# Performance work log

Hardware: AMD Instinct MI355X
Metric: run time of the kernel (lower is better)

The kernel has to match this reference:

```python
import jax, jax.numpy as jnp
import numpy as np

B, N, HID, HEADS, LAYERS, POOL = 2, 2048, 256, 4, 2, 128
D = HID // HEADS  # per-head dim


def attn_pool(x, w1, b1, w2, b2):
    # x: [B,N,HID]; mask is all-ones in this module's forward, so plain softmax
    s = jnp.tanh(x @ w1 + b1) @ w2 + b2            # [B,N]
    a = jax.nn.softmax(s, axis=-1)                  # [B,N]
    return jnp.einsum('bn,bnc->bc', a, x)           # [B,HID]


def gat_layer(x, adj_mask, proj_w, a_src, a_dst):
    # x: [B,N,HID] -> h: [B,N,HEADS,D]
    h = (x @ proj_w).reshape(x.shape[0], x.shape[1], HEADS, D)
    src = jnp.einsum('bnhd,hd->bnh', h, a_src)      # [B,N,H]
    dst = jnp.einsum('bnhd,hd->bnh', h, a_dst)      # [B,N,H]
    logits = src[:, :, None, :] + dst[:, None, :, :]  # [B,i,j,H]
    logits = jnp.where(logits >= 0, logits, 0.2 * logits)  # leaky_relu(0.2)
    logits = jnp.where(adj_mask[..., None], logits, jnp.float32(-1e9))
    attn = jax.nn.softmax(logits, axis=2)           # softmax over j (neighbors)
    out = jnp.einsum('bijh,bjhd->bihd', attn, h)
    return out.reshape(x.shape[0], x.shape[1], HEADS * D)


def setup_inputs() -> dict:
    key = jax.random.key(0)
    ks = jax.random.split(key, 16)
    sd = 0.05
    gene_expr = jax.random.normal(ks[0], (B, N), dtype=jnp.float32)
    gene_adj = jax.random.randint(ks[1], (B, N, N), 0, 2, dtype=jnp.int32)
    in_w = jax.random.normal(ks[2], (HID,), dtype=jnp.float32) * sd
    in_b = jax.random.normal(ks[3], (HID,), dtype=jnp.float32) * sd
    proj_w = jax.random.normal(ks[4], (LAYERS, HID, HID), dtype=jnp.float32) * sd
    attn_src = jax.random.normal(ks[5], (LAYERS, HEADS, D), dtype=jnp.float32) * sd
    attn_dst = jax.random.normal(ks[6], (LAYERS, HEADS, D), dtype=jnp.float32) * sd
    pool_w1 = jax.random.normal(ks[7], (LAYERS, HID, POOL), dtype=jnp.float32) * sd
    pool_b1 = jax.random.normal(ks[8], (LAYERS, POOL), dtype=jnp.float32) * sd
    pool_w2 = jax.random.normal(ks[9], (LAYERS, POOL), dtype=jnp.float32) * sd
    pool_b2 = jax.random.normal(ks[10], (LAYERS,), dtype=jnp.float32) * sd
    ip_w1 = jax.random.normal(ks[11], (HID, POOL), dtype=jnp.float32) * sd
    ip_b1 = jax.random.normal(ks[12], (POOL,), dtype=jnp.float32) * sd
    ip_w2 = jax.random.normal(ks[13], (POOL,), dtype=jnp.float32) * sd
    ip_b2 = jax.random.normal(ks[14], (), dtype=jnp.float32) * sd
    return dict(gene_expr=gene_expr, gene_adj=gene_adj, in_w=in_w, in_b=in_b,
                proj_w=proj_w, attn_src=attn_src, attn_dst=attn_dst,
                pool_w1=pool_w1, pool_b1=pool_b1, pool_w2=pool_w2, pool_b2=pool_b2,
                ip_w1=ip_w1, ip_b1=ip_b1, ip_w2=ip_w2, ip_b2=ip_b2)


def reference(gene_expr, gene_adj, in_w, in_b, proj_w, attn_src, attn_dst,
              pool_w1, pool_b1, pool_w2, pool_b2, ip_w1, ip_b1, ip_w2, ip_b2):
    # input_proj: Linear(1, HID) on gene_expr[...,None], then relu
    x = jax.nn.relu(gene_expr[:, :, None] * in_w + in_b)  # [B,N,HID]
    raw_pooled = attn_pool(x, ip_w1, ip_b1, ip_w2, ip_b2)
    adj_mask = gene_adj > 0
    node_outs, pooled_outs = [], []
    cur = x
    for l in range(LAYERS):
        cur = gat_layer(cur, adj_mask, proj_w[l], attn_src[l], attn_dst[l])
        cur = jax.nn.elu(cur)
        node_outs.append(cur)
        pooled_outs.append(attn_pool(cur, pool_w1[l], pool_b1[l], pool_w2[l], pool_b2[l]))
    # (raw_pooled, node_out_0, node_out_1, pooled_0, pooled_1); final_pooled == pooled_outs[-1]
    return (raw_pooled, *node_outs, *pooled_outs)
```

## Files before the change

### kernel.cpp

```cpp
#include <hip/hip_runtime.h>
#include <hip/hip_bf16.h>

#define B_ 2
#define N_ 2048
#define HID_ 256
#define HEADS_ 4
#define D_ 64
#define POOL_ 128
#define LOG2E_ 1.4426950408889634f

typedef __bf16 bf16;
typedef __bf16 bf16x8 __attribute__((ext_vector_type(8)));
typedef float f32x4 __attribute__((ext_vector_type(4)));

__device__ __forceinline__ float fast_tanh(float x) {
    x = fminf(fmaxf(x, -15.f), 15.f);
    float t = __expf(2.f * x);
    return (t - 1.f) / (t + 1.f);
}

__global__ void k_setup(const int* __restrict__ adj, unsigned* __restrict__ am,
                        const float* __restrict__ ge, const float* __restrict__ iw,
                        const float* __restrict__ ib, bf16* __restrict__ xb,
                        const float* __restrict__ proj_w, const float* __restrict__ ipw1,
                        const float* __restrict__ pw1, bf16* __restrict__ wT0,
                        bf16* __restrict__ wT1, bf16* __restrict__ ipw1T,
                        bf16* __restrict__ w1T0, bf16* __restrict__ w1T1) {
    int blk = blockIdx.x, tid = threadIdx.x;
    if (blk < 32768) {
        int gid = blk * 256 + tid;
        int v = adj[gid];
        unsigned long long mask = __ballot(v > 0);
        int lane = tid & 63;
        if (lane == 0) am[gid >> 5] = (unsigned)mask;
        else if (lane == 32) am[gid >> 5] = (unsigned)(mask >> 32);
    } else if (blk < 36864) {
        int row = blk - 32768;
        float g = ge[row];
        float v = fmaxf(g * iw[tid] + ib[tid], 0.f);
        xb[row * HID_ + tid] = (bf16)v;
    } else {
        int o = (blk - 36864) * 256 + tid;
        const float* src; bf16* dst; int Nc, loc;
        if (o < 65536)       { src = proj_w;         dst = wT0;   Nc = 256; loc = o; }
        else if (o < 131072) { src = proj_w + 65536; dst = wT1;   Nc = 256; loc = o - 65536; }
        else if (o < 163840) { src = ipw1;           dst = ipw1T; Nc = 128; loc = o - 131072; }
        else if (o < 196608) { src = pw1;            dst = w1T0;  Nc = 128; loc = o - 163840; }
        else                 { src = pw1 + 32768;    dst = w1T1;  Nc = 128; loc = o - 196608; }
        int n = loc >> 8, k = loc & 255;
        dst[loc] = (bf16)src[k * Nc + n];
    }
}

__device__ __forceinline__ void pool_sw_body(const bf16* __restrict__ A,
                                             const bf16* __restrict__ W1T,
                                             const float* __restrict__ b1,
                                             const float* __restrict__ w2,
                                             const float* __restrict__ b2,
                                             float* __restrict__ part,
                                             float* __restrict__ pz,
                                             int slot, int b, int ch, char* smemraw) {
    int n0 = ch * 16;
    int tid = threadIdx.x;
    int w = tid >> 6, lane = tid & 63, r = lane & 15, g = lane >> 4;
    const bf16* ap = A + ((long long)(b * N_ + n0) + r) * 256 + g * 8;
    f32x4 acc[2] = {{0,0,0,0},{0,0,0,0}};
    for (int ks = 0; ks < 256; ks += 32) {
        bf16x8 af = *(const bf16x8*)(ap + ks);
        #pragma unroll
        for (int nf = 0; nf < 2; ++nf) {
            bf16x8 bfr = *(const bf16x8*)(W1T + (w * 32 + nf * 16 + r) * 256 + ks + g * 8);
            acc[nf] = __builtin_amdgcn_mfma_f32_16x16x32_bf16(af, bfr, acc[nf], 0, 0, 0);
        }
    }
    float b1v[2], w2v[2];
    #pragma unroll
    for (int nf = 0; nf < 2; ++nf) {
        b1v[nf] = b1[w * 32 + nf * 16 + r];
        w2v[nf] = w2[w * 32 + nf * 16 + r];
    }
    float (*pred)[16] = (float (*)[16])smemraw;
    float* el = (float*)(smemraw + 256);
    #pragma unroll
    for (int q = 0; q < 4; ++q) {
        float p = fast_tanh(acc[0][q] + b1v[0]) * w2v[0] + fast_tanh(acc[1][q] + b1v[1]) * w2v[1];
        p += __shfl_xor(p, 1); p += __shfl_xor(p, 2);
        p += __shfl_xor(p, 4); p += __shfl_xor(p, 8);
        if (r == 0) pred[w][g * 4 + q] = p;
    }
    __syncthreads();
    if (tid < 16) {
        float s = pred[0][tid] + pred[1][tid] + pred[2][tid] + pred[3][tid] + b2[0];
        el[tid] = __expf(s);
    }
    __syncthreads();
    if (tid == 0) {
        float z = 0.f;
        #pragma unroll
        for (int n = 0; n < 16; ++n) z += el[n];
        pz[(slot * B_ + b) * 128 + ch] = z;
    }
    const bf16* xp = A + (long long)(b * N_ + n0) * 256 + tid;
    float accum = 0.f;
    #pragma unroll
    for (int n = 0; n < 16; ++n) accum += el[n] * (float)xp[n * 256];
    part[(((long long)slot * B_ + b) * 128 + ch) * 256 + tid] = accum;
}

__global__ __launch_bounds__(256) void k_gemm_h_pool(const bf16* __restrict__ A,
                                                     const bf16* __restrict__ WT,
                                                     const float* __restrict__ as,
                                                     const float* __restrict__ ad,
                                                     bf16* __restrict__ hbT,
                                                     float* __restrict__ srcM,
                                                     float* __restrict__ dstT,
                                                     const bf16* __restrict__ W1T,
                                                     const float* __restrict__ b1,
                                                     const float* __restrict__ w2,
                                                     const float* __restrict__ b2,
                                                     float* __restrict__ part,
                                                     float* __restrict__ pz, int slot) {
    __shared__ __align__(16) char smem[16640];
    int blk = blockIdx.x;
    if (blk >= 256) {
        int pb = blk - 256;
        pool_sw_body(A, W1T, b1, w2, b2, part, pz, slot, pb >> 7, pb & 127, smem);
        return;
    }
    int i0 = (blk & 63) * 64, hd = blk >> 6;
    int n0 = hd * 64;
    int w = threadIdx.x >> 6, lane = threadIdx.x & 63, r = lane & 15, g = lane >> 4;
    const bf16* ap = A + (i0 + w * 16 + r) * 256 + g * 8;
    f32x4 acc[4] = {{0,0,0,0},{0,0,0,0},{0,0,0,0},{0,0,0,0}};
    for (int ks = 0; ks < 256; ks += 32) {
        bf16x8 af = *(const bf16x8*)(ap + ks);
        #pragma unroll
        for (int nf = 0; nf < 4; ++nf) {
            bf16x8 bfr = *(const bf16x8*)(WT + (n0 + nf * 16 + r) * 256 + ks + g * 8);
            acc[nf] = __builtin_amdgcn_mfma_f32_16x16x32_bf16(af, bfr, acc[nf], 0, 0, 0);
        }
    }
    int b = i0 >> 11, nbase = i0 & 2047;
    int bh = b * HEADS_ + hd;
    float asv[4], adv[4];
    #pragma unroll
    for (int nf = 0; nf < 4; ++nf) {
        asv[nf] = as[hd * 64 + nf * 16 + r] * LOG2E_;
        adv[nf] = ad[hd * 64 + nf * 16 + r] * LOG2E_;
    }
    float (*tr)[65] = (float (*)[65])smem;
    #pragma unroll
    for (int q = 0; q < 4; ++q) {
        int ln = w * 16 + g * 4 + q;
        float ps = 0.f, pd = 0.f;
        #pragma unroll
        for (int nf = 0; nf < 4; ++nf) {
            float v = acc[nf][q];
            ps += v * asv[nf];
            pd += v * adv[nf];
            tr[nf * 16 + r][ln] = v;
        }
        ps += __shfl_xor(ps, 1); ps += __shfl_xor(ps, 2);
        ps += __shfl_xor(ps, 4); ps += __shfl_xor(ps, 8);
        pd += __shfl_xor(pd, 1); pd += __shfl_xor(pd, 2);
        pd += __shfl_xor(pd, 4); pd += __shfl_xor(pd, 8);
        if (r == 0) {
            srcM[bh * N_ + nbase + ln] = ps;
            dstT[bh * N_ + nbase + ln] = pd;
        }
    }
    __syncthreads();
    int ld = threadIdx.x >> 2, ln0 = (threadIdx.x & 3) * 16;
    bf16x8 o0, o1;
    #pragma unroll
    for (int e = 0; e < 8; ++e) {
        o0[e] = (bf16)tr[ld][ln0 + e];
        o1[e] = (bf16)tr[ld][ln0 + 8 + e];
    }
    bf16* hp = hbT + ((long long)bh * D_ + ld) * N_ + nbase + ln0;
    *(bf16x8*)(hp) = o0;
    *(bf16x8*)(hp + 8) = o1;
}

__global__ __launch_bounds__(256) void k_pool_sw(const bf16* __restrict__ A,
                                                 const bf16* __restrict__ W1T,
                                                 const float* __restrict__ b1,
                                                 const float* __restrict__ w2,
                                                 const float* __restrict__ b2,
                                                 float* __restrict__ part,
                                                 float* __restrict__ pz, int slot) {
    __shared__ __align__(16) char smem[320];
    pool_sw_body(A, W1T, b1, w2, b2, part, pz, slot, blockIdx.y, blockIdx.x, smem);
}

__global__ __launch_bounds__(512, 4) void k_attn(const float* __restrict__ srcM,
                                                 const float* __restrict__ dstT,
                                                 const unsigned* __restrict__ am,
                                                 const bf16* __restrict__ hbT,
                                                 float* __restrict__ nodeOut,
                                                 bf16* __restrict__ xbNext) {
    int it = blockIdx.x, hd = blockIdx.y, b = blockIdx.z;
    int i0 = it * 32;
    int tid = threadIdx.x;
    int w = tid >> 6, lane = tid & 63, r = lane & 15, g = lane >> 4;
    int rg = w >> 2, wj = w & 3;
    int bh = b * HEADS_ + hd;
    const float* drow = dstT + bh * N_;
    const bf16* vbase = hbT + (long long)bh * D_ * N_;

    __shared__ __align__(16) char smem[34816];
    bf16* vt = (bf16*)smem;
    float (*accs)[16][68] = (float (*)[16][68])smem;
    __shared__ float lred[8][16];

    int i = i0 + rg * 16 + r;
    const unsigned* mrow = am + ((long long)(b * N_ + i)) * 64;
    float sv = srcM[bh * N_ + i];

    f32x4 acc[4] = {{0,0,0,0},{0,0,0,0},{0,0,0,0},{0,0,0,0}};
    float l = 0.f;

    bf16x8 st[4];
    #pragma unroll
    for (int k = 0; k < 4; ++k) {
        int s = tid + k * 512, d = s >> 5, seg = s & 31;
        st[k] = *(const bf16x8*)(vbase + d * N_ + seg * 8);
    }

    #pragma unroll
    for (int t = 0; t < 8; ++t) {
        #pragma unroll
        for (int k = 0; k < 4; ++k) {
            int s = tid + k * 512, d = s >> 5, seg = s & 31;
            *(bf16x8*)(vt + d * 264 + seg * 8) = st[k];
        }
        __syncthreads();
        if (t < 7) {
            #pragma unroll
            for (int k = 0; k < 4; ++k) {
                int s = tid + k * 512, d = s >> 5, seg = s & 31;
                st[k] = *(const bf16x8*)(vbase + d * N_ + (t + 1) * 256 + seg * 8);
            }
        }
        #pragma unroll
        for (int s = 0; s < 2; ++s) {
            int jb = t * 256 + wj * 64 + s * 32 + g * 8;
            float4 dv0 = *(const float4*)(drow + jb);
            float4 dv1 = *(const float4*)(drow + jb + 4);
            unsigned mb = (mrow[t * 8 + wj * 2 + s] >> (g * 8)) & 0xFFu;
            float dd[8] = {dv0.x, dv0.y, dv0.z, dv0.w, dv1.x, dv1.y, dv1.z, dv1.w};
            bf16x8 af;
            float es[8];
            #pragma unroll
            for (int tt = 0; tt < 8; ++tt) {
                float s2 = sv + dd[tt];
                float lv = fmaxf(s2, 0.2f * s2);
                float e2 = exp2f(lv);
                e2 = ((mb >> tt) & 1u) ? e2 : 0.f;
                es[tt] = e2;
                af[tt] = (bf16)e2;
            }
            l += ((es[0] + es[1]) + (es[2] + es[3])) + ((es[4] + es[5]) + (es[6] + es[7]));
            #pragma unroll
            for (int nf = 0; nf < 4; ++nf) {
                bf16x8 vf = *(const bf16x8*)(vt + (nf * 16 + r) * 264 + wj * 64 + s * 32 + g * 8);
                acc[nf] = __builtin_amdgcn_mfma_f32_16x16x32_bf16(af, vf, acc[nf], 0, 0, 0);
            }
        }
        __syncthreads();
    }

    l += __shfl_xor(l, 16);
    l += __shfl_xor(l, 32);
    if (g == 0) lred[w][r] = l;
    #pragma unroll
    for (int nf = 0; nf < 4; ++nf)
        #pragma unroll
        for (int q = 0; q < 4; ++q)
            accs[w][g * 4 + q][nf * 16 + r] = acc[nf][q];
    __syncthreads();

    int cc = lane;
    #pragma unroll
    for (int k = 0; k < 4; ++k) {
        int rr = w * 4 + k;
        int rg2 = rr >> 4, rl = rr & 15;
        float ls = 0.f, v = 0.f;
        #pragma unroll
        for (int w2 = 0; w2 < 4; ++w2) {
            ls += lred[rg2 * 4 + w2][rl];
            v += accs[rg2 * 4 + w2][rl][cc];
        }
        v /= ls;
        float o = v > 0.f ? v : expm1f(v);
        int idx = (b * N_ + i0 + rr) * HID_ + hd * D_ + cc;
        nodeOut[idx] = o;
        xbNext[idx] = (bf16)o;
    }
}

__global__ __launch_bounds__(256) void k_pool_finals(const float* __restrict__ part,
                                                     const float* __restrict__ pz,
                                                     float* __restrict__ outRaw,
                                                     float* __restrict__ pool0,
                                                     float* __restrict__ pool1) {
    int slot = blockIdx.x >> 1, b = blockIdx.x & 1;
    int tid = threadIdx.x;
    int lane = tid & 63, w = tid >> 6;
    float z = (tid < 128) ? pz[(slot * B_ + b) * 128 + tid] : 0.f;
    #pragma unroll
    for (int o = 1; o < 64; o <<= 1) z += __shfl_xor(z, o);
    __shared__ float red[4];
    if (lane == 0) red[w] = z;
    __syncthreads();
    float Z = red[0] + red[1] + red[2] + red[3];
    float acc = 0.f;
    #pragma unroll 8
    for (int ch = 0; ch < 128; ++ch)
        acc += part[(((long long)slot * B_ + b) * 128 + ch) * 256 + tid];
    float* out = slot == 0 ? outRaw : (slot == 1 ? pool0 : pool1);
    out[b * HID_ + tid] = acc / Z;
}

extern "C" void kernel_launch(void* const* d_in, const int* in_sizes, int n_in,
                              void* d_out, int out_size, void* d_ws, size_t ws_size,
                              hipStream_t stream) {
    const float* ge     = (const float*)d_in[0];
    const int*   adj    = (const int*)d_in[1];
    const float* in_w   = (const float*)d_in[2];
    const float* in_b   = (const float*)d_in[3];
    const float* proj_w = (const float*)d_in[4];
    const float* a_src  = (const float*)d_in[5];
    const float* a_dst  = (const float*)d_in[6];
    const float* pw1    = (const float*)d_in[7];
    const float* pb1    = (const float*)d_in[8];
    const float* pw2    = (const float*)d_in[9];
    const float* pb2    = (const float*)d_in[10];
    const float* ipw1   = (const float*)d_in[11];
    const float* ipb1   = (const float*)d_in[12];
    const float* ipw2   = (const float*)d_in[13];
    const float* ipb2   = (const float*)d_in[14];

    char* ws = (char*)d_ws;
    bf16*     xb    = (bf16*)(ws + 0);
    bf16*     hbT   = (bf16*)(ws + 2097152);
    float*    srcM  = (float*)(ws + 4194304);
    float*    dstT  = (float*)(ws + 4259840);
    unsigned* am    = (unsigned*)(ws + 4325376);
    bf16*     wT0   = (bf16*)(ws + 5373952);
    bf16*     wT1   = wT0 + 65536;
    bf16*     ipw1T = wT1 + 65536;
    bf16*     w1T0  = ipw1T + 32768;
    bf16*     w1T1  = w1T0 + 32768;
    float*    part  = (float*)(ws + 5832704);
    float*    pz    = (float*)(ws + 6619136);

    float* outRaw = (float*)d_out;
    float* node0  = outRaw + 512;
    float* node1  = node0 + 1048576;
    float* pool0  = node1 + 1048576;
    float* pool1  = pool0 + 512;

    k_setup<<<37760, 256, 0, stream>>>(adj, am, ge, in_w, in_b, xb,
                                       proj_w, ipw1, pw1, wT0, wT1, ipw1T, w1T0, w1T1);

    k_gemm_h_pool<<<512, 256, 0, stream>>>(xb, wT0, a_src, a_dst, hbT, srcM, dstT,
                                           ipw1T, ipb1, ipw2, ipb2, part, pz, 0);
    k_attn<<<dim3(64, 4, 2), 512, 0, stream>>>(srcM, dstT, am, hbT, node0, xb);

    k_gemm_h_pool<<<512, 256, 0, stream>>>(xb, wT1, a_src + 256, a_dst + 256, hbT, srcM, dstT,
                                           w1T0, pb1, pw2, pb2, part, pz, 1);
    k_attn<<<dim3(64, 4, 2), 512, 0, stream>>>(srcM, dstT, am, hbT, node1, xb);

    k_pool_sw<<<dim3(128, B_), 256, 0, stream>>>(xb, w1T1, pb1 + POOL_, pw2 + 1, pb2 + 1,
                                                 part, pz, 2);
    k_pool_finals<<<6, 256, 0, stream>>>(part, pz, outRaw, pool0, pool1);
}
```

Baseline: 111.4 us.

## Restructure GAT attention: 16-row blocks, per-wave j-split, direct global V loads

```diff
diff --git a/kernel.cpp b/kernel.cpp
--- a/kernel.cpp
+++ b/kernel.cpp
@@ -193,85 +193,68 @@
     pool_sw_body(A, W1T, b1, w2, b2, part, pz, slot, blockIdx.y, blockIdx.x, smem);
 }
 
-__global__ __launch_bounds__(512, 4) void k_attn(const float* __restrict__ srcM,
+__global__ __launch_bounds__(512, 8) void k_attn(const float* __restrict__ srcM,
                                                  const float* __restrict__ dstT,
                                                  const unsigned* __restrict__ am,
                                                  const bf16* __restrict__ hbT,
                                                  float* __restrict__ nodeOut,
                                                  bf16* __restrict__ xbNext) {
     int it = blockIdx.x, hd = blockIdx.y, b = blockIdx.z;
-    int i0 = it * 32;
+    int i0 = it * 16;
     int tid = threadIdx.x;
     int w = tid >> 6, lane = tid & 63, r = lane & 15, g = lane >> 4;
-    int rg = w >> 2, wj = w & 3;
     int bh = b * HEADS_ + hd;
     const float* drow = dstT + bh * N_;
     const bf16* vbase = hbT + (long long)bh * D_ * N_;
 
     __shared__ __align__(16) char smem[34816];
-    bf16* vt = (bf16*)smem;
+    float* dls = (float*)smem;
     float (*accs)[16][68] = (float (*)[16][68])smem;
     __shared__ float lred[8][16];
 
-    int i = i0 + rg * 16 + r;
-    const unsigned* mrow = am + ((long long)(b * N_ + i)) * 64;
+    *(float4*)(dls + tid * 4) = *(const float4*)(drow + tid * 4);
+
+    int i = i0 + r;
+    const unsigned* mrow = am + ((long long)(b * N_ + i)) * 64 + w * 8;
+    uint4 m0 = *(const uint4*)(mrow);
+    uint4 m1 = *(const uint4*)(mrow + 4);
+    unsigned mw[8] = {m0.x, m0.y, m0.z, m0.w, m1.x, m1.y, m1.z, m1.w};
     float sv = srcM[bh * N_ + i];
 
     f32x4 acc[4] = {{0,0,0,0},{0,0,0,0},{0,0,0,0},{0,0,0,0}};
     float l = 0.f;
-
-    bf16x8 st[4];
-    #pragma unroll
-    for (int k = 0; k < 4; ++k) {
-        int s = tid + k * 512, d = s >> 5, seg = s & 31;
-        st[k] = *(const bf16x8*)(vbase + d * N_ + seg * 8);
-    }
-
-    #pragma unroll
-    for (int t = 0; t < 8; ++t) {
-        #pragma unroll
-        for (int k = 0; k < 4; ++k) {
-            int s = tid + k * 512, d = s >> 5, seg = s & 31;
-            *(bf16x8*)(vt + d * 264 + seg * 8) = st[k];
-        }
-        __syncthreads();
-        if (t < 7) {
-            #pragma unroll
-            for (int k = 0; k < 4; ++k) {
-                int s = tid + k * 512, d = s >> 5, seg = s & 31;
-                st[k] = *(const bf16x8*)(vbase + d * N_ + (t + 1) * 256 + seg * 8);
-            }
-        }
-        #pragma unroll
-        for (int s = 0; s < 2; ++s) {
-            int jb = t * 256 + wj * 64 + s * 32 + g * 8;
-            float4 dv0 = *(const float4*)(drow + jb);
-            float4 dv1 = *(const float4*)(drow + jb + 4);
-            unsigned mb = (mrow[t * 8 + wj * 2 + s] >> (g * 8)) & 0xFFu;
-            float dd[8] = {dv0.x, dv0.y, dv0.z, dv0.w, dv1.x, dv1.y, dv1.z, dv1.w};
-            bf16x8 af;
-            float es[8];
-            #pragma unroll
-            for (int tt = 0; tt < 8; ++tt) {
-                float s2 = sv + dd[tt];
-                float lv = fmaxf(s2, 0.2f * s2);
-                float e2 = exp2f(lv);
-                e2 = ((mb >> tt) & 1u) ? e2 : 0.f;
-                es[tt] = e2;
-                af[tt] = (bf16)e2;
-            }
-            l += ((es[0] + es[1]) + (es[2] + es[3])) + ((es[4] + es[5]) + (es[6] + es[7]));
-            #pragma unroll
-            for (int nf = 0; nf < 4; ++nf) {
-                bf16x8 vf = *(const bf16x8*)(vt + (nf * 16 + r) * 264 + wj * 64 + s * 32 + g * 8);
-                acc[nf] = __builtin_amdgcn_mfma_f32_16x16x32_bf16(af, vf, acc[nf], 0, 0, 0);
-            }
-        }
-        __syncthreads();
-    }
-
+    int jbase = w * 256;
+
+    __syncthreads();
+
+    #pragma unroll
+    for (int js = 0; js < 8; ++js) {
+        int jb = jbase + js * 32 + g * 8;
+        float4 dv0 = *(const float4*)(dls + jb);
+        float4 dv1 = *(const float4*)(dls + jb + 4);
+        unsigned mb = (mw[js] >> (g * 8)) & 0xFFu;
+        float dd[8] = {dv0.x, dv0.y, dv0.z, dv0.w, dv1.x, dv1.y, dv1.z, dv1.w};
+        bf16x8 af;
+        float es[8];
+        #pragma unroll
+        for (int t = 0; t < 8; ++t) {
+            float tt = sv + dd[t];
+            float lv = fmaxf(tt, 0.2f * tt);
+            float e2 = __builtin_amdgcn_exp2f(lv);
+            e2 = ((mb >> t) & 1u) ? e2 : 0.f;
+            es[t] = e2;
+            af[t] = (bf16)e2;
+        }
+        l += ((es[0] + es[1]) + (es[2] + es[3])) + ((es[4] + es[5]) + (es[6] + es[7]));
+        #pragma unroll
+        for (int nf = 0; nf < 4; ++nf) {
+            bf16x8 vf = *(const bf16x8*)(vbase + (nf * 16 + r) * N_ + jb);
+            acc[nf] = __builtin_amdgcn_mfma_f32_16x16x32_bf16(af, vf, acc[nf], 0, 0, 0);
+        }
+    }
     l += __shfl_xor(l, 16);
     l += __shfl_xor(l, 32);
+    __syncthreads();
     if (g == 0) lred[w][r] = l;
     #pragma unroll
     for (int nf = 0; nf < 4; ++nf)
@@ -282,14 +265,13 @@
 
     int cc = lane;
     #pragma unroll
-    for (int k = 0; k < 4; ++k) {
-        int rr = w * 4 + k;
-        int rg2 = rr >> 4, rl = rr & 15;
+    for (int k = 0; k < 2; ++k) {
+        int rr = w * 2 + k;
         float ls = 0.f, v = 0.f;
         #pragma unroll
-        for (int w2 = 0; w2 < 4; ++w2) {
-            ls += lred[rg2 * 4 + w2][rl];
-            v += accs[rg2 * 4 + w2][rl][cc];
+        for (int w2 = 0; w2 < 8; ++w2) {
+            ls += lred[w2][rr];
+            v += accs[w2][rr][cc];
         }
         v /= ls;
         float o = v > 0.f ? v : expm1f(v);
@@ -366,11 +348,11 @@
 
     k_gemm_h_pool<<<512, 256, 0, stream>>>(xb, wT0, a_src, a_dst, hbT, srcM, dstT,
                                            ipw1T, ipb1, ipw2, ipb2, part, pz, 0);
-    k_attn<<<dim3(64, 4, 2), 512, 0, stream>>>(srcM, dstT, am, hbT, node0, xb);
+    k_attn<<<dim3(128, 4, 2), 512, 0, stream>>>(srcM, dstT, am, hbT, node0, xb);
 
     k_gemm_h_pool<<<512, 256, 0, stream>>>(xb, wT1, a_src + 256, a_dst + 256, hbT, srcM, dstT,
                                            w1T0, pb1, pw2, pb2, part, pz, 1);
-    k_attn<<<dim3(64, 4, 2), 512, 0, stream>>>(srcM, dstT, am, hbT, node1, xb);
+    k_attn<<<dim3(128, 4, 2), 512, 0, stream>>>(srcM, dstT, am, hbT, node1, xb);
 
     k_pool_sw<<<dim3(128, B_), 256, 0, stream>>>(xb, w1T1, pb1 + POOL_, pw2 + 1, pb2 + 1,
                                                  part, pz, 2);
```

After: 123.4 us. 10.8% more time.

## Double k_attn block to 1024 threads splitting neighbor tiles across 8 waves

Applied to the files above, without the earlier changes.

```diff
diff --git a/kernel.cpp b/kernel.cpp
--- a/kernel.cpp
+++ b/kernel.cpp
@@ -193,17 +193,17 @@
     pool_sw_body(A, W1T, b1, w2, b2, part, pz, slot, blockIdx.y, blockIdx.x, smem);
 }
 
-__global__ __launch_bounds__(512, 4) void k_attn(const float* __restrict__ srcM,
-                                                 const float* __restrict__ dstT,
-                                                 const unsigned* __restrict__ am,
-                                                 const bf16* __restrict__ hbT,
-                                                 float* __restrict__ nodeOut,
-                                                 bf16* __restrict__ xbNext) {
+__global__ __launch_bounds__(1024, 8) void k_attn(const float* __restrict__ srcM,
+                                                  const float* __restrict__ dstT,
+                                                  const unsigned* __restrict__ am,
+                                                  const bf16* __restrict__ hbT,
+                                                  float* __restrict__ nodeOut,
+                                                  bf16* __restrict__ xbNext) {
     int it = blockIdx.x, hd = blockIdx.y, b = blockIdx.z;
     int i0 = it * 32;
     int tid = threadIdx.x;
     int w = tid >> 6, lane = tid & 63, r = lane & 15, g = lane >> 4;
-    int rg = w >> 2, wj = w & 3;
+    int rg = w >> 3, wj = w & 7;
     int bh = b * HEADS_ + hd;
     const float* drow = dstT + bh * N_;
     const bf16* vbase = hbT + (long long)bh * D_ * N_;
@@ -211,61 +211,61 @@
     __shared__ __align__(16) char smem[34816];
     bf16* vt = (bf16*)smem;
     float (*accs)[16][68] = (float (*)[16][68])smem;
-    __shared__ float lred[8][16];
+    __shared__ float lred[16][16];
 
     int i = i0 + rg * 16 + r;
     const unsigned* mrow = am + ((long long)(b * N_ + i)) * 64;
+    unsigned mw[8];
+    #pragma unroll
+    for (int t = 0; t < 8; ++t) mw[t] = mrow[t * 8 + wj];
     float sv = srcM[bh * N_ + i];
 
     f32x4 acc[4] = {{0,0,0,0},{0,0,0,0},{0,0,0,0},{0,0,0,0}};
     float l = 0.f;
 
-    bf16x8 st[4];
-    #pragma unroll
-    for (int k = 0; k < 4; ++k) {
-        int s = tid + k * 512, d = s >> 5, seg = s & 31;
+    bf16x8 st[2];
+    #pragma unroll
+    for (int k = 0; k < 2; ++k) {
+        int s = tid + k * 1024, d = s >> 5, seg = s & 31;
         st[k] = *(const bf16x8*)(vbase + d * N_ + seg * 8);
     }
 
     #pragma unroll
     for (int t = 0; t < 8; ++t) {
         #pragma unroll
-        for (int k = 0; k < 4; ++k) {
-            int s = tid + k * 512, d = s >> 5, seg = s & 31;
+        for (int k = 0; k < 2; ++k) {
+            int s = tid + k * 1024, d = s >> 5, seg = s & 31;
             *(bf16x8*)(vt + d * 264 + seg * 8) = st[k];
         }
         __syncthreads();
         if (t < 7) {
             #pragma unroll
-            for (int k = 0; k < 4; ++k) {
-                int s = tid + k * 512, d = s >> 5, seg = s & 31;
+            for (int k = 0; k < 2; ++k) {
+                int s = tid + k * 1024, d = s >> 5, seg = s & 31;
                 st[k] = *(const bf16x8*)(vbase + d * N_ + (t + 1) * 256 + seg * 8);
             }
         }
-        #pragma unroll
-        for (int s = 0; s < 2; ++s) {
-            int jb = t * 256 + wj * 64 + s * 32 + g * 8;
-            float4 dv0 = *(const float4*)(drow + jb);
-            float4 dv1 = *(const float4*)(drow + jb + 4);
-            unsigned mb = (mrow[t * 8 + wj * 2 + s] >> (g * 8)) & 0xFFu;
-            float dd[8] = {dv0.x, dv0.y, dv0.z, dv0.w, dv1.x, dv1.y, dv1.z, dv1.w};
-            bf16x8 af;
-            float es[8];
-            #pragma unroll
-            for (int tt = 0; tt < 8; ++tt) {
-                float s2 = sv + dd[tt];
-                float lv = fmaxf(s2, 0.2f * s2);
-                float e2 = exp2f(lv);
-                e2 = ((mb >> tt) & 1u) ? e2 : 0.f;
-                es[tt] = e2;
-                af[tt] = (bf16)e2;
-            }
-            l += ((es[0] + es[1]) + (es[2] + es[3])) + ((es[4] + es[5]) + (es[6] + es[7]));
-            #pragma unroll
-            for (int nf = 0; nf < 4; ++nf) {
-                bf16x8 vf = *(const bf16x8*)(vt + (nf * 16 + r) * 264 + wj * 64 + s * 32 + g * 8);
-                acc[nf] = __builtin_amdgcn_mfma_f32_16x16x32_bf16(af, vf, acc[nf], 0, 0, 0);
-            }
+        int jb = t * 256 + wj * 32 + g * 8;
+        float4 dv0 = *(const float4*)(drow + jb);
+        float4 dv1 = *(const float4*)(drow + jb + 4);
+        unsigned mb = (mw[t] >> (g * 8)) & 0xFFu;
+        float dd[8] = {dv0.x, dv0.y, dv0.z, dv0.w, dv1.x, dv1.y, dv1.z, dv1.w};
+        bf16x8 af;
+        float es[8];
+        #pragma unroll
+        for (int tt = 0; tt < 8; ++tt) {
+            float s2 = sv + dd[tt];
+            float lv = fmaxf(s2, 0.2f * s2);
+            float e2 = __builtin_amdgcn_exp2f(lv);
+            e2 = ((mb >> tt) & 1u) ? e2 : 0.f;
+            es[tt] = e2;
+            af[tt] = (bf16)e2;
+        }
+        l += ((es[0] + es[1]) + (es[2] + es[3])) + ((es[4] + es[5]) + (es[6] + es[7]));
+        #pragma unroll
+        for (int nf = 0; nf < 4; ++nf) {
+            bf16x8 vf = *(const bf16x8*)(vt + (nf * 16 + r) * 264 + wj * 32 + g * 8);
+            acc[nf] = __builtin_amdgcn_mfma_f32_16x16x32_bf16(af, vf, acc[nf], 0, 0, 0);
         }
         __syncthreads();
     }
@@ -273,29 +273,33 @@
     l += __shfl_xor(l, 16);
     l += __shfl_xor(l, 32);
     if (g == 0) lred[w][r] = l;
-    #pragma unroll
-    for (int nf = 0; nf < 4; ++nf)
-        #pragma unroll
-        for (int q = 0; q < 4; ++q)
-            accs[w][g * 4 + q][nf * 16 + r] = acc[nf][q];
-    __syncthreads();
-
-    int cc = lane;
-    #pragma unroll
-    for (int k = 0; k < 4; ++k) {
-        int rr = w * 4 + k;
-        int rg2 = rr >> 4, rl = rr & 15;
-        float ls = 0.f, v = 0.f;
-        #pragma unroll
-        for (int w2 = 0; w2 < 4; ++w2) {
-            ls += lred[rg2 * 4 + w2][rl];
-            v += accs[rg2 * 4 + w2][rl][cc];
-        }
-        v /= ls;
-        float o = v > 0.f ? v : expm1f(v);
-        int idx = (b * N_ + i0 + rr) * HID_ + hd * D_ + cc;
-        nodeOut[idx] = o;
-        xbNext[idx] = (bf16)o;
+
+    #pragma unroll
+    for (int ph = 0; ph < 2; ++ph) {
+        if (rg == ph) {
+            #pragma unroll
+            for (int nf = 0; nf < 4; ++nf)
+                #pragma unroll
+                for (int q = 0; q < 4; ++q)
+                    accs[wj][g * 4 + q][nf * 16 + r] = acc[nf][q];
+        }
+        __syncthreads();
+        {
+            int rr = tid >> 6;
+            int cc = tid & 63;
+            float ls = 0.f, v = 0.f;
+            #pragma unroll
+            for (int w2 = 0; w2 < 8; ++w2) {
+                ls += lred[ph * 8 + w2][rr];
+                v += accs[w2][rr][cc];
+            }
+            v /= ls;
+            float o = v > 0.f ? v : expm1f(v);
+            int idx = (b * N_ + i0 + ph * 16 + rr) * HID_ + hd * D_ + cc;
+            nodeOut[idx] = o;
+            xbNext[idx] = (bf16)o;
+        }
+        __syncthreads();
     }
 }
 
@@ -366,11 +370,11 @@
 
     k_gemm_h_pool<<<512, 256, 0, stream>>>(xb, wT0, a_src, a_dst, hbT, srcM, dstT,
                                            ipw1T, ipb1, ipw2, ipb2, part, pz, 0);
-    k_attn<<<dim3(64, 4, 2), 512, 0, stream>>>(srcM, dstT, am, hbT, node0, xb);
+    k_attn<<<dim3(64, 4, 2), 1024, 0, stream>>>(srcM, dstT, am, hbT, node0, xb);
 
     k_gemm_h_pool<<<512, 256, 0, stream>>>(xb, wT1, a_src + 256, a_dst + 256, hbT, srcM, dstT,
                                            w1T0, pb1, pw2, pb2, part, pz, 1);
-    k_attn<<<dim3(64, 4, 2), 512, 0, stream>>>(srcM, dstT, am, hbT, node1, xb);
+    k_attn<<<dim3(64, 4, 2), 1024, 0, stream>>>(srcM, dstT, am, hbT, node1, xb);
 
     k_pool_sw<<<dim3(128, B_), 256, 0, stream>>>(xb, w1T1, pb1 + POOL_, pw2 + 1, pb2 + 1,
                                                  part, pz, 2);
```

New measurement: 104.8 us. 1.06x faster.
